# Optimization experiments

Hardware: AMD Instinct MI355X
Metric: run time of the kernel (lower is better)

Reference implementation:

```python
import jax, jax.numpy as jnp
import numpy as np

B, S, D = 2, 2048, 2048
QH, KVH, HD = 32, 8, 64
GRP = QH // KVH  # GQA group size = 4


def setup_inputs() -> dict:
    key = jax.random.key(0)
    ks = jax.random.split(key, 9)
    x = jax.random.normal(ks[0], (B, S, D), jnp.float32)
    # RoPE angle table: [S, HD//2] -> stacked (cos, sin) -> [S, HD//2, 2]
    inv_freq = 1.0 / (10000.0 ** (np.arange(0, HD, 2, dtype=np.float32) / HD))
    ang = np.arange(S, dtype=np.float32)[:, None] * inv_freq[None, :]
    freqs = jnp.stack([jnp.cos(jnp.asarray(ang)), jnp.sin(jnp.asarray(ang))], axis=-1).astype(jnp.float32)
    w = 0.02
    Wq = jax.random.normal(ks[1], (D, QH * HD), jnp.float32) * w
    bq = jnp.zeros((QH * HD,), jnp.float32)
    Wk = jax.random.normal(ks[2], (D, KVH * HD), jnp.float32) * w
    bk = jnp.zeros((KVH * HD,), jnp.float32)
    Wv = jax.random.normal(ks[3], (D, KVH * HD), jnp.float32) * w
    bv = jnp.zeros((KVH * HD,), jnp.float32)
    Wo = jax.random.normal(ks[4], (QH * HD, D), jnp.float32) * w
    bo = jnp.zeros((D,), jnp.float32)
    return {"x": x, "freqs": freqs, "Wq": Wq, "bq": bq, "Wk": Wk, "bk": bk,
            "Wv": Wv, "bv": bv, "Wo": Wo, "bo": bo}


def _rope(xh, cos, sin):
    # xh: [b, s, h, hd]; complex rotation on adjacent pairs, like view_as_complex
    b, s, h, hd = xh.shape
    xp = xh.reshape(b, s, h, hd // 2, 2)
    x0, x1 = xp[..., 0], xp[..., 1]
    o0 = x0 * cos - x1 * sin
    o1 = x0 * sin + x1 * cos
    return jnp.stack([o0, o1], axis=-1).reshape(b, s, h, hd)


def reference(x, freqs, Wq, bq, Wk, bk, Wv, bv, Wo, bo):
    b, s, _ = x.shape
    q = (x @ Wq + bq).reshape(b, s, QH, HD)
    k = (x @ Wk + bk).reshape(b, s, KVH, HD)
    v = (x @ Wv + bv).reshape(b, s, KVH, HD)
    cos = freqs[:s, :, 0][None, :, None, :]  # [1, s, 1, hd//2]
    sin = freqs[:s, :, 1][None, :, None, :]
    q = _rope(q, cos, sin)
    k = _rope(k, cos, sin)
    # [b, h, s, hd]
    q = q.transpose(0, 2, 1, 3).reshape(b, KVH, GRP, s, HD)
    k = k.transpose(0, 2, 1, 3)  # [b, kvh, s, hd]
    v = v.transpose(0, 2, 1, 3)
    scores = jnp.einsum('bkgsh,bkth->bkgst', q, k) / jnp.sqrt(jnp.float32(HD))
    attn = jax.nn.softmax(scores, axis=-1)
    o = jnp.einsum('bkgst,bkth->bkgsh', attn, v)  # [b, kvh, grp, s, hd]
    o = o.reshape(b, QH, s, HD).transpose(0, 2, 1, 3).reshape(b, s, QH * HD)
    return o @ Wo + bo
```

## Files before the change

### kernel.cpp

```cpp
#include <hip/hip_runtime.h>
#include <stdint.h>

#define B_   2
#define S_   2048
#define D_   2048
#define QH_  32
#define KVH_ 8
#define HD_  64

typedef short  short8  __attribute__((ext_vector_type(8)));
typedef float  floatx4 __attribute__((ext_vector_type(4)));

__device__ __forceinline__ ushort f2b(float f) {
  union { float f; uint32_t u; } c; c.f = f;
  uint32_t u = c.u;
  return (ushort)((u + 0x7FFFu + ((u >> 16) & 1u)) >> 16);
}

__device__ __forceinline__ uint32_t fbits(float f) {
  union { float f; uint32_t u; } c; c.f = f;
  return c.u;
}

__device__ __forceinline__ short8 mk8(uint32_t a, uint32_t b, uint32_t c, uint32_t d) {
  union { uint4 u; short8 s; } v; v.u = (uint4){a, b, c, d}; return v.s;
}

__device__ __forceinline__ uint32_t cvtpk(float a, float b) {
  uint32_t r;
  asm("v_cvt_pk_bf16_f32 %0, %1, %2" : "=v"(r) : "v"(a), "v"(b));
  return r;
}

__device__ __forceinline__ void dma16(const void* g, void* l) {
  __builtin_amdgcn_global_load_lds(
      (const __attribute__((address_space(1))) uint32_t*)(uintptr_t)g,
      (__attribute__((address_space(3))) uint32_t*)(uintptr_t)l, 16, 0, 0);
}

#define QSCALE 0.18033688f


__global__ __launch_bounds__(256) void conv_x_kernel(const float* __restrict__ X,
                                                     ushort* __restrict__ Xb) {
  size_t i = ((size_t)blockIdx.x * 256 + threadIdx.x) * 4;
  float4 v = *(const float4*)(X + i);
  ushort4 o;
  o.x = f2b(v.x); o.y = f2b(v.y); o.z = f2b(v.z); o.w = f2b(v.w);
  *(ushort4*)(Xb + i) = o;
}

__global__ void tconv_all_kernel(const float* __restrict__ Wq, const float* __restrict__ Wk,
                                 const float* __restrict__ Wv, const float* __restrict__ Wo,
                                 ushort* __restrict__ wqkv, ushort* __restrict__ wo) {
  __shared__ float tile[32][33];
  int z = blockIdx.z;
  const float* W; ushort* Wt; int N;
  if (z == 0)      { W = Wq; Wt = wqkv;                        N = 2048; }
  else if (z == 1) { W = Wk; Wt = wqkv + (size_t)2048 * 2048;  N = 512;  }
  else if (z == 2) { W = Wv; Wt = wqkv + (size_t)2560 * 2048;  N = 512;  }
  else             { W = Wo; Wt = wo;                          N = 2048; }
  int bx = blockIdx.x, by = blockIdx.y;
  if (bx * 32 >= N) return;
  int tx = threadIdx.x, ty = threadIdx.y;
#pragma unroll
  for (int i = 0; i < 32; i += 8)
    tile[ty + i][tx] = W[(size_t)(by * 32 + ty + i) * N + bx * 32 + tx];
  __syncthreads();
#pragma unroll
  for (int i = 0; i < 32; i += 8)
    Wt[(size_t)(bx * 32 + ty + i) * 2048 + by * 32 + tx] = f2b(tile[tx][ty + i]);
}

__global__ void bias_kernel(const float* __restrict__ bq, const float* __restrict__ bk,
                            const float* __restrict__ bv, float* __restrict__ outb) {
  int i = blockIdx.x * 256 + threadIdx.x;
  if (i >= 3072) return;
  float v;
  if (i < 2048)      v = bq[i];
  else if (i < 2560) v = bk[i - 2048];
  else               v = bv[i - 2560];
  outb[i] = v;
}


__global__ __launch_bounds__(256) void gemm_qkv_kernel(
    const ushort* __restrict__ A, const ushort* __restrict__ Bt,
    const float* __restrict__ bias, const float2* __restrict__ F2,
    ushort* __restrict__ qb, ushort* __restrict__ kb, ushort* __restrict__ vb) {
  const int K = 2048;
  __shared__ ushort sA[2][128 * 32];
  __shared__ ushort sB[2][128 * 32];
  const int tid  = threadIdx.x;
  const int bm   = blockIdx.y, bn = blockIdx.x;
  const int wave = tid >> 6, lane = tid & 63;
  const int quad = lane >> 4, l16 = lane & 15;
  const int wm   = (wave >> 1) * 64, wn = (wave & 1) * 64;

  const ushort* Ab = A  + (size_t)(bm * 128) * K;
  const ushort* Bb = Bt + (size_t)(bn * 128) * K;

  const int gr = lane >> 2;
  const int gu = (lane & 3) * 8;

  floatx4 acc[4][4];
#pragma unroll
  for (int i = 0; i < 4; i++)
#pragma unroll
    for (int j = 0; j < 4; j++) acc[i][j] = (floatx4){0.f, 0.f, 0.f, 0.f};

#pragma unroll
  for (int j = 0; j < 2; j++) {
    int row = j * 64 + wave * 16 + gr;
    dma16(Ab + (size_t)row * K + gu, &sA[0][j * 2048 + wave * 512]);
    dma16(Bb + (size_t)row * K + gu, &sB[0][j * 2048 + wave * 512]);
  }

  int cur = 0;
  for (int k0 = 0; k0 < K; k0 += 32) {
    __syncthreads();
    if (k0 + 32 < K) {
      int nxt = cur ^ 1;
#pragma unroll
      for (int j = 0; j < 2; j++) {
        int row = j * 64 + wave * 16 + gr;
        dma16(Ab + (size_t)row * K + k0 + 32 + gu, &sA[nxt][j * 2048 + wave * 512]);
        dma16(Bb + (size_t)row * K + k0 + 32 + gu, &sB[nxt][j * 2048 + wave * 512]);
      }
    }
    short8 af[4], bf[4];
#pragma unroll
    for (int mi = 0; mi < 4; mi++)
      af[mi] = *(const short8*)&sA[cur][(wm + mi * 16 + l16) * 32 + quad * 8];
#pragma unroll
    for (int ni = 0; ni < 4; ni++)
      bf[ni] = *(const short8*)&sB[cur][(wn + ni * 16 + l16) * 32 + quad * 8];
#pragma unroll
    for (int mi = 0; mi < 4; mi++)
#pragma unroll
      for (int ni = 0; ni < 4; ni++)
        acc[mi][ni] = __builtin_amdgcn_mfma_f32_16x16x32_bf16(
            af[mi], bf[ni], acc[mi][ni], 0, 0, 0);
    cur ^= 1;
  }

  const int isQ = (bn < 16);
  const int isV = (bn >= 20);
  const int hh  = wn >> 6;
  const float sySign = (l16 & 1) ? 1.f : -1.f;
  ushort* dst;
  int hbase;
  if (isQ)      { dst = qb; hbase = bn * 2 + hh; }
  else if (!isV){ dst = kb; hbase = (bn - 16) * 2 + hh; }
  else          { dst = vb; hbase = (bn - 20) * 2 + hh; }
  const int NH = isQ ? QH_ : KVH_;

  float bvv[4];
#pragma unroll
  for (int ni = 0; ni < 4; ni++)
    bvv[ni] = bias[bn * 128 + wn + ni * 16 + l16];

#pragma unroll
  for (int mi = 0; mi < 4; mi++) {
#pragma unroll
    for (int r = 0; r < 4; r++) {
      int row = bm * 128 + wm + mi * 16 + quad * 4 + r;
      int s = row & 2047, bb = row >> 11;
      size_t base = (((size_t)bb * NH + hbase) * S_ + s) * HD_ + l16 * 4;
      ushort4 pk;
      if (!isV) {
        float o[4];
#pragma unroll
        for (int ni = 0; ni < 4; ni++) {
          float xv = acc[mi][ni][r] + bvv[ni];
          float2 cs = F2[s * 32 + ni * 8 + (l16 >> 1)];
          float pp = __shfl_xor(xv, 1);
          float oo = fmaf(pp * sySign, cs.y, xv * cs.x);
          if (isQ) oo *= QSCALE;
          o[ni] = oo;
        }
        pk.x = f2b(o[0]); pk.y = f2b(o[1]); pk.z = f2b(o[2]); pk.w = f2b(o[3]);
      } else {
        pk.x = f2b(acc[mi][0][r] + bvv[0]);
        pk.y = f2b(acc[mi][1][r] + bvv[1]);
        pk.z = f2b(acc[mi][2][r] + bvv[2]);
        pk.w = f2b(acc[mi][3][r] + bvv[3]);
      }
      *(ushort4*)&dst[base] = pk;
    }
  }
}


__global__ __launch_bounds__(256) void gemm_bt_kernel(
    const ushort* __restrict__ A, const ushort* __restrict__ Bt,
    const float* __restrict__ bias, float* __restrict__ C,
    int M, int N, int K) {
  __shared__ ushort sA[2][128 * 32];
  __shared__ ushort sB[2][128 * 32];
  const int tid  = threadIdx.x;
  const int bm   = blockIdx.y, bn = blockIdx.x;
  const int wave = tid >> 6, lane = tid & 63;
  const int quad = lane >> 4, l16 = lane & 15;
  const int wm   = (wave >> 1) * 64, wn = (wave & 1) * 64;

  const ushort* Ab = A  + (size_t)(bm * 128) * K;
  const ushort* Bb = Bt + (size_t)(bn * 128) * K;

  const int gr = lane >> 2;
  const int gu = (lane & 3) * 8;

  floatx4 acc[4][4];
#pragma unroll
  for (int i = 0; i < 4; i++)
#pragma unroll
    for (int j = 0; j < 4; j++) acc[i][j] = (floatx4){0.f, 0.f, 0.f, 0.f};

#pragma unroll
  for (int j = 0; j < 2; j++) {
    int row = j * 64 + wave * 16 + gr;
    dma16(Ab + (size_t)row * K + gu, &sA[0][j * 2048 + wave * 512]);
    dma16(Bb + (size_t)row * K + gu, &sB[0][j * 2048 + wave * 512]);
  }

  int cur = 0;
  for (int k0 = 0; k0 < K; k0 += 32) {
    __syncthreads();
    if (k0 + 32 < K) {
      int nxt = cur ^ 1;
#pragma unroll
      for (int j = 0; j < 2; j++) {
        int row = j * 64 + wave * 16 + gr;
        dma16(Ab + (size_t)row * K + k0 + 32 + gu, &sA[nxt][j * 2048 + wave * 512]);
        dma16(Bb + (size_t)row * K + k0 + 32 + gu, &sB[nxt][j * 2048 + wave * 512]);
      }
    }
    short8 af[4], bf[4];
#pragma unroll
    for (int mi = 0; mi < 4; mi++)
      af[mi] = *(const short8*)&sA[cur][(wm + mi * 16 + l16) * 32 + quad * 8];
#pragma unroll
    for (int ni = 0; ni < 4; ni++)
      bf[ni] = *(const short8*)&sB[cur][(wn + ni * 16 + l16) * 32 + quad * 8];
#pragma unroll
    for (int mi = 0; mi < 4; mi++)
#pragma unroll
      for (int ni = 0; ni < 4; ni++)
        acc[mi][ni] = __builtin_amdgcn_mfma_f32_16x16x32_bf16(
            af[mi], bf[ni], acc[mi][ni], 0, 0, 0);
    cur ^= 1;
  }

#pragma unroll
  for (int mi = 0; mi < 4; mi++) {
#pragma unroll
    for (int ni = 0; ni < 4; ni++) {
      int col  = bn * 128 + wn + ni * 16 + l16;
      float bv = bias[col];
#pragma unroll
      for (int r = 0; r < 4; r++) {
        int row = bm * 128 + wm + mi * 16 + quad * 4 + r;
        C[(size_t)row * N + col] = acc[mi][ni][r] + bv;
      }
    }
  }
}


__global__ void vpack_kernel(const ushort* __restrict__ vb, ushort* __restrict__ Vt) {
  __shared__ ushort tile[64][65];
  int s0 = blockIdx.x * 64;
  int bh = blockIdx.y;
  int tx = threadIdx.x, ty = threadIdx.y;
  int pc = (tx & 32) | ((tx & 12) << 1) | ((tx & 16) >> 2) | (tx & 3);
#pragma unroll
  for (int i = 0; i < 64; i += 8)
    tile[ty + i][tx] = vb[((size_t)bh * S_ + s0 + ty + i) * HD_ + tx];
  __syncthreads();
#pragma unroll
  for (int i = 0; i < 64; i += 8) {
    int dp = ty + i;
    int dt = (dp & 3) * 16 + (dp >> 2);
    Vt[((size_t)bh * HD_ + dt) * S_ + s0 + pc] = tile[tx][dp];
  }
}


__global__ __launch_bounds__(512, 4) void attn_kernel(
    const ushort* __restrict__ Q, const ushort* __restrict__ K,
    const ushort* __restrict__ Vt, ushort* __restrict__ O) {
  const int id  = blockIdx.x + 8 * (blockIdx.y + 32 * blockIdx.z);
  const int kvh = id & 7;
  const int qt  = (id >> 3) & 7;
  const int qh  = kvh * 4 + ((id >> 6) & 3);
  const int b   = id >> 8;
  const int tid = threadIdx.x;
  const int wave = tid >> 6, lane = tid & 63;
  const int quad = lane >> 4, l16 = lane & 15;

  __shared__ ushort kBuf[2][64 * 64];
  __shared__ ushort vBuf[2][64 * 64];

  const ushort* Qh = Q  + ((size_t)(b * QH_ + qh)) * S_ * HD_;
  const ushort* Kh = K  + ((size_t)(b * KVH_ + kvh)) * S_ * HD_;
  const ushort* Vh = Vt + ((size_t)(b * KVH_ + kvh)) * HD_ * S_;

  const int dr = lane >> 3;
  const int du = (lane & 7) ^ (dr & 7);
  const size_t kLaneOff = (size_t)(wave * 8 + dr) * 64 + du * 8;
  const size_t vLaneOff = (size_t)(wave * 8 + dr) * S_ + du * 8;
  const int swz = l16 & 7;

  const int q0 = qt * 256 + wave * 32;
  short8 aq[2][2];
#pragma unroll
  for (int m = 0; m < 2; m++)
#pragma unroll
    for (int s2 = 0; s2 < 2; s2++)
      aq[m][s2] = *(const short8*)(Qh + (size_t)(q0 + m * 16 + l16) * HD_ + s2 * 32 + quad * 8);

  floatx4 oacc[2][4];
#pragma unroll
  for (int m = 0; m < 2; m++)
#pragma unroll
    for (int t = 0; t < 4; t++) oacc[m][t] = (floatx4){0.f, 0.f, 0.f, 0.f};
  float ls[2] = {0.f, 0.f};

  dma16(Kh + kLaneOff, &kBuf[0][wave * 512]);
  dma16(Vh + vLaneOff, &vBuf[0][wave * 512]);

  int cur = 0;
  for (int kv0 = 0; kv0 < S_; kv0 += 64) {
    __syncthreads();
    if (kv0 + 64 < S_) {
      int nxt = cur ^ 1;
      dma16(Kh + (size_t)(kv0 + 64) * 64 + kLaneOff, &kBuf[nxt][wave * 512]);
      dma16(Vh + (size_t)(kv0 + 64) + vLaneOff,      &vBuf[nxt][wave * 512]);
    }

#pragma unroll
    for (int u = 0; u < 2; u++) {
      uint32_t pk[2][4];
#pragma unroll
      for (int cc = 0; cc < 2; cc++) {
        const int c = u * 2 + cc;
        short8 kf0 = *(const short8*)&kBuf[cur][(c * 16 + l16) * 64 + ((quad ^ swz) * 8)];
        short8 kf1 = *(const short8*)&kBuf[cur][(c * 16 + l16) * 64 + (((4 + quad) ^ swz) * 8)];
#pragma unroll
        for (int m = 0; m < 2; m++) {
          floatx4 sc = (floatx4){0.f, 0.f, 0.f, 0.f};
          __builtin_amdgcn_s_setprio(1);
          sc = __builtin_amdgcn_mfma_f32_16x16x32_bf16(kf0, aq[m][0], sc, 0, 0, 0);
          sc = __builtin_amdgcn_mfma_f32_16x16x32_bf16(kf1, aq[m][1], sc, 0, 0, 0);
          __builtin_amdgcn_s_setprio(0);
          float p0 = __builtin_amdgcn_exp2f(sc[0]);
          float p1 = __builtin_amdgcn_exp2f(sc[1]);
          float p2 = __builtin_amdgcn_exp2f(sc[2]);
          float p3 = __builtin_amdgcn_exp2f(sc[3]);
          ls[m] += (p0 + p1) + (p2 + p3);
          pk[m][cc * 2 + 0] = cvtpk(p0, p1);
          pk[m][cc * 2 + 1] = cvtpk(p2, p3);
        }
      }
#pragma unroll
      for (int t = 0; t < 4; t++) {
        const int row = (t * 16 + l16) * 64;
        short8 vf = *(const short8*)&vBuf[cur][row + (((u * 4 + quad) ^ swz) * 8)];
        __builtin_amdgcn_s_setprio(1);
#pragma unroll
        for (int m = 0; m < 2; m++) {
          short8 ap = mk8(pk[m][0], pk[m][1], pk[m][2], pk[m][3]);
          oacc[m][t] = __builtin_amdgcn_mfma_f32_16x16x32_bf16(ap, vf, oacc[m][t], 0, 0, 0);
        }
        __builtin_amdgcn_s_setprio(0);
      }
    }
    cur ^= 1;
  }

#pragma unroll
  for (int m = 0; m < 2; m++) {
    ls[m] += __shfl_xor(ls[m], 16);
    ls[m] += __shfl_xor(ls[m], 32);
  }
#pragma unroll
  for (int m = 0; m < 2; m++) {
#pragma unroll
    for (int r = 0; r < 4; r++) {
      float l = __shfl(ls[m], (lane & 48) | (quad * 4 + r));
      float inv = 1.0f / l;
      int srow = q0 + m * 16 + quad * 4 + r;
      size_t base = ((size_t)b * S_ + srow) * (QH_ * HD_) + (size_t)qh * HD_;
#pragma unroll
      for (int t = 0; t < 4; t++)
        O[base + t * 16 + l16] = f2b(oacc[m][t][r] * inv);
    }
  }
}


extern "C" void kernel_launch(void* const* d_in, const int* in_sizes, int n_in,
                              void* d_out, int out_size, void* d_ws, size_t ws_size,
                              hipStream_t stream) {
  const float* x  = (const float*)d_in[0];
  const float* fr = (const float*)d_in[1];
  const float* Wq = (const float*)d_in[2];
  const float* bq = (const float*)d_in[3];
  const float* Wk = (const float*)d_in[4];
  const float* bk = (const float*)d_in[5];
  const float* Wv = (const float*)d_in[6];
  const float* bv = (const float*)d_in[7];
  const float* Wo = (const float*)d_in[8];
  const float* bo = (const float*)d_in[9];
  float* out = (float*)d_out;
  char* ws = (char*)d_ws;

  ushort* xb    = (ushort*)(ws + 0);
  ushort* wqkv  = (ushort*)(ws + 16777216);
  ushort* wo    = (ushort*)(ws + 29360128);
  float*  biasq = (float* )(ws + 37748736);
  ushort* qb    = (ushort*)(ws + 37761024);
  ushort* kb    = (ushort*)(ws + 54538240);
  ushort* vb    = (ushort*)(ws + 58732544);
  ushort* vt    = (ushort*)(ws + 62926848);
  ushort* ob    = xb;

  conv_x_kernel<<<8192, 256, 0, stream>>>(x, xb);
  tconv_all_kernel<<<dim3(64, 64, 4), dim3(32, 8), 0, stream>>>(Wq, Wk, Wv, Wo, wqkv, wo);
  bias_kernel<<<12, 256, 0, stream>>>(bq, bk, bv, biasq);

  gemm_qkv_kernel<<<dim3(3072 / 128, 4096 / 128), 256, 0, stream>>>(
      xb, wqkv, biasq, (const float2*)fr, qb, kb, vb);

  vpack_kernel<<<dim3(2048 / 64, 16), dim3(64, 8), 0, stream>>>(vb, vt);

  attn_kernel<<<dim3(8, 32, 2), 512, 0, stream>>>(qb, kb, vt, ob);

  gemm_bt_kernel<<<dim3(2048 / 128, 4096 / 128), 256, 0, stream>>>(
      ob, wo, bo, out, 4096, 2048, 2048);
}
```

Measured before the change: 316.1 us.

## Restructure QKV GEMM as 256x256 tile with phased, swizzled LDS pipeline

The QKV projection GEMM now computes a 256x256 output tile per 512-thread block instead of 128x128 per 256-thread block, with K-step 64. Its main loop is an eight-phase schedule that interleaves global-to-LDS DMA for upcoming tiles with MFMA work, using explicit barriers, vmcnt waits and setprio. LDS accesses use an XOR swizzle to avoid bank conflicts. The epilogue is remapped to the new wave layout and writes ushort2 pairs. The goals are more data reuse per block and better overlap of memory and compute, at the cost of more LDS (128 KB), much higher register pressure, and only 192 blocks, which may leave CUs underfilled.

```diff
diff --git a/kernel.cpp b/kernel.cpp
--- a/kernel.cpp
+++ b/kernel.cpp
@@ -84,109 +84,182 @@
 }
 
 
-__global__ __launch_bounds__(256) void gemm_qkv_kernel(
+__global__ __launch_bounds__(512, 2) void gemm_qkv_kernel(
     const ushort* __restrict__ A, const ushort* __restrict__ Bt,
     const float* __restrict__ bias, const float2* __restrict__ F2,
     ushort* __restrict__ qb, ushort* __restrict__ kb, ushort* __restrict__ vb) {
   const int K = 2048;
-  __shared__ ushort sA[2][128 * 32];
-  __shared__ ushort sB[2][128 * 32];
+  __shared__ ushort sA[2][256 * 64];
+  __shared__ ushort sB[2][256 * 64];
   const int tid  = threadIdx.x;
   const int bm   = blockIdx.y, bn = blockIdx.x;
   const int wave = tid >> 6, lane = tid & 63;
   const int quad = lane >> 4, l16 = lane & 15;
-  const int wm   = (wave >> 1) * 64, wn = (wave & 1) * 64;
-
-  const ushort* Ab = A  + (size_t)(bm * 128) * K;
-  const ushort* Bb = Bt + (size_t)(bn * 128) * K;
-
-  const int gr = lane >> 2;
-  const int gu = (lane & 3) * 8;
-
-  floatx4 acc[4][4];
-#pragma unroll
-  for (int i = 0; i < 4; i++)
+  const int wm2  = wave >> 2, wn4 = wave & 3;
+  const int sw7  = l16 & 7;
+  const int dr   = lane >> 3, du = (lane & 7) ^ dr;
+  const int srow = wave * 8 + dr;
+  const int lcol = (lane & 7) * 8;
+
+  const ushort* Ab = A  + (size_t)(bm * 256) * K;
+  const ushort* Bb = Bt + (size_t)(bn * 256) * K;
+
+  floatx4 acc[8][4];
+#pragma unroll
+  for (int i = 0; i < 8; i++)
 #pragma unroll
     for (int j = 0; j < 4; j++) acc[i][j] = (floatx4){0.f, 0.f, 0.f, 0.f};
 
-#pragma unroll
-  for (int j = 0; j < 2; j++) {
-    int row = j * 64 + wave * 16 + gr;
-    dma16(Ab + (size_t)row * K + gu, &sA[0][j * 2048 + wave * 512]);
-    dma16(Bb + (size_t)row * K + gu, &sB[0][j * 2048 + wave * 512]);
-  }
-
-  int cur = 0;
-  for (int k0 = 0; k0 < K; k0 += 32) {
-    __syncthreads();
-    if (k0 + 32 < K) {
-      int nxt = cur ^ 1;
-#pragma unroll
-      for (int j = 0; j < 2; j++) {
-        int row = j * 64 + wave * 16 + gr;
-        dma16(Ab + (size_t)row * K + k0 + 32 + gu, &sA[nxt][j * 2048 + wave * 512]);
-        dma16(Bb + (size_t)row * K + k0 + 32 + gu, &sB[nxt][j * 2048 + wave * 512]);
-      }
-    }
-    short8 af[4], bf[4];
-#pragma unroll
-    for (int mi = 0; mi < 4; mi++)
-      af[mi] = *(const short8*)&sA[cur][(wm + mi * 16 + l16) * 32 + quad * 8];
-#pragma unroll
-    for (int ni = 0; ni < 4; ni++)
-      bf[ni] = *(const short8*)&sB[cur][(wn + ni * 16 + l16) * 32 + quad * 8];
-#pragma unroll
-    for (int mi = 0; mi < 4; mi++)
-#pragma unroll
-      for (int ni = 0; ni < 4; ni++)
-        acc[mi][ni] = __builtin_amdgcn_mfma_f32_16x16x32_bf16(
-            af[mi], bf[ni], acc[mi][ni], 0, 0, 0);
-    cur ^= 1;
-  }
-
-  const int isQ = (bn < 16);
-  const int isV = (bn >= 20);
-  const int hh  = wn >> 6;
+  short8 af[4][2], bf[4][2];
+
+#define STG_A(t, h) do {                                                      \
+    dma16(Ab + (size_t)((h)*128 +      srow) * 2048 + (size_t)(t)*64 + du*8,  \
+          &sA[(t)&1][((h)*128 +      srow) * 64 + lcol]);                     \
+    dma16(Ab + (size_t)((h)*128 + 64 + srow) * 2048 + (size_t)(t)*64 + du*8,  \
+          &sA[(t)&1][((h)*128 + 64 + srow) * 64 + lcol]);                     \
+  } while (0)
+
+#define STG_B(t, h) do {                                                      \
+    dma16(Bb + (size_t)((h)*128 +      srow) * 2048 + (size_t)(t)*64 + du*8,  \
+          &sB[(t)&1][((h)*128 +      srow) * 64 + lcol]);                     \
+    dma16(Bb + (size_t)((h)*128 + 64 + srow) * 2048 + (size_t)(t)*64 + du*8,  \
+          &sB[(t)&1][((h)*128 + 64 + srow) * 64 + lcol]);                     \
+  } while (0)
+
+#define LDA(Sb, mh) do {                                                      \
+    _Pragma("unroll") for (int mi2 = 0; mi2 < 4; mi2++) {                     \
+      const int rr = ((mh)*128 + wm2*64 + mi2*16 + l16) * 64;                 \
+      af[mi2][0] = *(const short8*)&(Sb)[rr + (((quad    ) ^ sw7) * 8)];      \
+      af[mi2][1] = *(const short8*)&(Sb)[rr + (((quad + 4) ^ sw7) * 8)];      \
+    } } while (0)
+
+#define LDB(Sb, nh) do {                                                      \
+    _Pragma("unroll") for (int ni2 = 0; ni2 < 2; ni2++) {                     \
+      const int rr = ((nh)*128 + wn4*32 + ni2*16 + l16) * 64;                 \
+      bf[(nh)*2+ni2][0] = *(const short8*)&(Sb)[rr + (((quad    ) ^ sw7) * 8)]; \
+      bf[(nh)*2+ni2][1] = *(const short8*)&(Sb)[rr + (((quad + 4) ^ sw7) * 8)]; \
+    } } while (0)
+
+#define MFMA_PH(mh, nh) do {                                                  \
+    __builtin_amdgcn_s_setprio(1);                                           \
+    _Pragma("unroll") for (int mi2 = 0; mi2 < 4; mi2++)                       \
+    _Pragma("unroll") for (int ni2 = 0; ni2 < 2; ni2++)                       \
+    _Pragma("unroll") for (int ks = 0; ks < 2; ks++)                          \
+      acc[(mh)*4+mi2][(nh)*2+ni2] = __builtin_amdgcn_mfma_f32_16x16x32_bf16(  \
+        af[mi2][ks], bf[(nh)*2+ni2][ks], acc[(mh)*4+mi2][(nh)*2+ni2], 0,0,0); \
+    __builtin_amdgcn_s_setprio(0);                                            \
+  } while (0)
+
+#define PH_SYNC() do {                                                        \
+    __builtin_amdgcn_sched_barrier(0);                                        \
+    __builtin_amdgcn_s_barrier();                                             \
+    asm volatile("s_waitcnt lgkmcnt(0)" ::: "memory");                        \
+    __builtin_amdgcn_sched_barrier(0);                                        \
+  } while (0)
+
+#define PH_END() do {                                                         \
+    __builtin_amdgcn_sched_barrier(0);                                        \
+    __builtin_amdgcn_s_barrier();                                             \
+    __builtin_amdgcn_sched_barrier(0);                                        \
+  } while (0)
+
+  STG_A(0, 0); STG_A(0, 1); STG_B(0, 0); STG_B(0, 1);
+  STG_A(1, 0); STG_B(1, 0); STG_B(1, 1);
+  asm volatile("s_waitcnt vmcnt(6)" ::: "memory");
+  __builtin_amdgcn_s_barrier();
+
+#pragma unroll 1
+  for (int i = 0; i < 16; ++i) {
+    const int t0 = 2 * i, t1 = 2 * i + 1;
+    const bool more = (i < 15);
+    const ushort* A0 = sA[0]; const ushort* B0 = sB[0];
+    const ushort* A1 = sA[1]; const ushort* B1 = sB[1];
+
+    LDB(B0, 0); LDA(A0, 0);
+    STG_A(t1, 1);
+    PH_SYNC(); MFMA_PH(0, 0); PH_END();
+
+    LDB(B0, 1);
+    if (more) STG_A(t0 + 2, 0);
+    PH_SYNC(); MFMA_PH(0, 1); PH_END();
+
+    LDA(A0, 1);
+    if (more) STG_B(t0 + 2, 0);
+    PH_SYNC(); MFMA_PH(1, 0); PH_END();
+
+    if (more) STG_B(t0 + 2, 1);
+    PH_SYNC(); MFMA_PH(1, 1);
+    if (more) asm volatile("s_waitcnt vmcnt(6)" ::: "memory");
+    else      asm volatile("s_waitcnt vmcnt(0)" ::: "memory");
+    PH_END();
+
+    LDB(B1, 0); LDA(A1, 0);
+    if (more) STG_A(t0 + 2, 1);
+    PH_SYNC(); MFMA_PH(0, 0); PH_END();
+
+    LDB(B1, 1);
+    if (more) STG_A(t1 + 2, 0);
+    PH_SYNC(); MFMA_PH(0, 1); PH_END();
+
+    LDA(A1, 1);
+    if (more) STG_B(t1 + 2, 0);
+    PH_SYNC(); MFMA_PH(1, 0); PH_END();
+
+    if (more) STG_B(t1 + 2, 1);
+    PH_SYNC(); MFMA_PH(1, 1);
+    if (more) asm volatile("s_waitcnt vmcnt(6)" ::: "memory");
+    PH_END();
+  }
+
+#undef STG_A
+#undef STG_B
+#undef LDA
+#undef LDB
+#undef MFMA_PH
+#undef PH_SYNC
+#undef PH_END
+
+  const int isQ = (bn < 8);
+  const int isV = (bn >= 10);
+  ushort* dst = isQ ? qb : (isV ? vb : kb);
+  const int NH   = isQ ? QH_ : KVH_;
+  const int hoff = isQ ? 0 : (isV ? 10 : 8);
   const float sySign = (l16 & 1) ? 1.f : -1.f;
-  ushort* dst;
-  int hbase;
-  if (isQ)      { dst = qb; hbase = bn * 2 + hh; }
-  else if (!isV){ dst = kb; hbase = (bn - 16) * 2 + hh; }
-  else          { dst = vb; hbase = (bn - 20) * 2 + hh; }
-  const int NH = isQ ? QH_ : KVH_;
+  const int dpb = l16 * 4 + (wn4 & 1) * 2;
 
   float bvv[4];
 #pragma unroll
   for (int ni = 0; ni < 4; ni++)
-    bvv[ni] = bias[bn * 128 + wn + ni * 16 + l16];
-
-#pragma unroll
-  for (int mi = 0; mi < 4; mi++) {
+    bvv[ni] = bias[bn * 256 + (ni >> 1) * 128 + wn4 * 32 + (ni & 1) * 16 + l16];
+
+#pragma unroll
+  for (int mi = 0; mi < 8; mi++) {
 #pragma unroll
     for (int r = 0; r < 4; r++) {
-      int row = bm * 128 + wm + mi * 16 + quad * 4 + r;
+      int row = bm * 256 + (mi >> 2) * 128 + wm2 * 64 + (mi & 3) * 16 + quad * 4 + r;
       int s = row & 2047, bb = row >> 11;
-      size_t base = (((size_t)bb * NH + hbase) * S_ + s) * HD_ + l16 * 4;
-      ushort4 pk;
+      float o[4];
       if (!isV) {
-        float o[4];
 #pragma unroll
         for (int ni = 0; ni < 4; ni++) {
           float xv = acc[mi][ni][r] + bvv[ni];
-          float2 cs = F2[s * 32 + ni * 8 + (l16 >> 1)];
+          float2 cs = F2[s * 32 + (wn4 & 1) * 16 + (ni & 1) * 8 + (l16 >> 1)];
           float pp = __shfl_xor(xv, 1);
           float oo = fmaf(pp * sySign, cs.y, xv * cs.x);
           if (isQ) oo *= QSCALE;
           o[ni] = oo;
         }
-        pk.x = f2b(o[0]); pk.y = f2b(o[1]); pk.z = f2b(o[2]); pk.w = f2b(o[3]);
       } else {
-        pk.x = f2b(acc[mi][0][r] + bvv[0]);
-        pk.y = f2b(acc[mi][1][r] + bvv[1]);
-        pk.z = f2b(acc[mi][2][r] + bvv[2]);
-        pk.w = f2b(acc[mi][3][r] + bvv[3]);
+#pragma unroll
+        for (int ni = 0; ni < 4; ni++) o[ni] = acc[mi][ni][r] + bvv[ni];
       }
-      *(ushort4*)&dst[base] = pk;
+#pragma unroll
+      for (int hh = 0; hh < 2; hh++) {
+        int h = (bn - hoff) * 4 + hh * 2 + (wn4 >> 1);
+        size_t base = (((size_t)bb * NH + h) * S_ + s) * HD_ + dpb;
+        ushort2 st; st.x = f2b(o[hh * 2 + 0]); st.y = f2b(o[hh * 2 + 1]);
+        *(ushort2*)&dst[base] = st;
+      }
     }
   }
 }
@@ -429,7 +502,7 @@
   tconv_all_kernel<<<dim3(64, 64, 4), dim3(32, 8), 0, stream>>>(Wq, Wk, Wv, Wo, wqkv, wo);
   bias_kernel<<<12, 256, 0, stream>>>(bq, bk, bv, biasq);
 
-  gemm_qkv_kernel<<<dim3(3072 / 128, 4096 / 128), 256, 0, stream>>>(
+  gemm_qkv_kernel<<<dim3(3072 / 256, 4096 / 256), 512, 0, stream>>>(
       xb, wqkv, biasq, (const float2*)fr, qb, kb, vb);
 
   vpack_kernel<<<dim3(2048 / 64, 16), dim3(64, 8), 0, stream>>>(vb, vt);
```

Result: faster. 309.6 us (-2.0%).

## Fuse V transpose and bias gather into QKV GEMM epilogue; batch attention score MFMAs

Applied to the files above, without the earlier changes.

The QKV GEMM epilogue now writes V straight into the permuted transposed layout the attention kernel reads, so the separate vpack kernel and the intermediate V buffer go away. Biases are read directly from bq/bk/bv, which removes the bias-copy kernel. In the attention loop, all score MFMAs for a 64-key tile are issued together under one priority raise before the exp and PV phases, giving longer MFMA runs. The cost is more live registers for the score fragments and strided, narrow stores in the V epilogue.

```diff
diff --git a/kernel.cpp b/kernel.cpp
--- a/kernel.cpp
+++ b/kernel.cpp
@@ -72,22 +72,12 @@
     Wt[(size_t)(bx * 32 + ty + i) * 2048 + by * 32 + tx] = f2b(tile[tx][ty + i]);
 }
 
-__global__ void bias_kernel(const float* __restrict__ bq, const float* __restrict__ bk,
-                            const float* __restrict__ bv, float* __restrict__ outb) {
-  int i = blockIdx.x * 256 + threadIdx.x;
-  if (i >= 3072) return;
-  float v;
-  if (i < 2048)      v = bq[i];
-  else if (i < 2560) v = bk[i - 2048];
-  else               v = bv[i - 2560];
-  outb[i] = v;
-}
-
 
 __global__ __launch_bounds__(256) void gemm_qkv_kernel(
     const ushort* __restrict__ A, const ushort* __restrict__ Bt,
-    const float* __restrict__ bias, const float2* __restrict__ F2,
-    ushort* __restrict__ qb, ushort* __restrict__ kb, ushort* __restrict__ vb) {
+    const float* __restrict__ bq, const float* __restrict__ bk,
+    const float* __restrict__ bv, const float2* __restrict__ F2,
+    ushort* __restrict__ qb, ushort* __restrict__ kb, ushort* __restrict__ vt) {
   const int K = 2048;
   __shared__ ushort sA[2][128 * 32];
   __shared__ ushort sB[2][128 * 32];
@@ -148,27 +138,26 @@
   const int isV = (bn >= 20);
   const int hh  = wn >> 6;
   const float sySign = (l16 & 1) ? 1.f : -1.f;
-  ushort* dst;
-  int hbase;
-  if (isQ)      { dst = qb; hbase = bn * 2 + hh; }
-  else if (!isV){ dst = kb; hbase = (bn - 16) * 2 + hh; }
-  else          { dst = vb; hbase = (bn - 20) * 2 + hh; }
-  const int NH = isQ ? QH_ : KVH_;
+
+  const float* bsrc = isQ ? bq : (isV ? bv : bk);
+  const int    boff = isQ ? 0  : (isV ? 2560 : 2048);
 
   float bvv[4];
 #pragma unroll
   for (int ni = 0; ni < 4; ni++)
-    bvv[ni] = bias[bn * 128 + wn + ni * 16 + l16];
-
-#pragma unroll
-  for (int mi = 0; mi < 4; mi++) {
-#pragma unroll
-    for (int r = 0; r < 4; r++) {
-      int row = bm * 128 + wm + mi * 16 + quad * 4 + r;
-      int s = row & 2047, bb = row >> 11;
-      size_t base = (((size_t)bb * NH + hbase) * S_ + s) * HD_ + l16 * 4;
-      ushort4 pk;
-      if (!isV) {
+    bvv[ni] = bsrc[bn * 128 + wn + ni * 16 + l16 - boff];
+
+  if (!isV) {
+    ushort* dst = isQ ? qb : kb;
+    const int NH    = isQ ? QH_ : KVH_;
+    const int hbase = isQ ? (bn * 2 + hh) : ((bn - 16) * 2 + hh);
+#pragma unroll
+    for (int mi = 0; mi < 4; mi++) {
+#pragma unroll
+      for (int r = 0; r < 4; r++) {
+        int row = bm * 128 + wm + mi * 16 + quad * 4 + r;
+        int s = row & 2047, bb = row >> 11;
+        size_t base = (((size_t)bb * NH + hbase) * S_ + s) * HD_ + l16 * 4;
         float o[4];
 #pragma unroll
         for (int ni = 0; ni < 4; ni++) {
@@ -179,14 +168,28 @@
           if (isQ) oo *= QSCALE;
           o[ni] = oo;
         }
+        ushort4 pk;
         pk.x = f2b(o[0]); pk.y = f2b(o[1]); pk.z = f2b(o[2]); pk.w = f2b(o[3]);
-      } else {
-        pk.x = f2b(acc[mi][0][r] + bvv[0]);
-        pk.y = f2b(acc[mi][1][r] + bvv[1]);
-        pk.z = f2b(acc[mi][2][r] + bvv[2]);
-        pk.w = f2b(acc[mi][3][r] + bvv[3]);
-      }
-      *(ushort4*)&dst[base] = pk;
+        *(ushort4*)&dst[base] = pk;
+      }
+    }
+  } else {
+    const int h = (bn - 20) * 2 + hh;
+#pragma unroll
+    for (int mi = 0; mi < 4; mi++) {
+      int row0 = bm * 128 + wm + mi * 16 + quad * 4;
+      int bb   = row0 >> 11;
+      int posb = ((row0 & 2047) & ~63) + (mi & 2) * 16 + quad * 8 + (mi & 1) * 4;
+#pragma unroll
+      for (int ni = 0; ni < 4; ni++) {
+        int dt = ni * 16 + l16;
+        ushort4 st;
+        st.x = f2b(acc[mi][ni][0] + bvv[ni]);
+        st.y = f2b(acc[mi][ni][1] + bvv[ni]);
+        st.z = f2b(acc[mi][ni][2] + bvv[ni]);
+        st.w = f2b(acc[mi][ni][3] + bvv[ni]);
+        *(ushort4*)&vt[(((size_t)bb * 8 + h) * 64 + dt) * (size_t)S_ + posb] = st;
+      }
     }
   }
 }
@@ -267,25 +270,6 @@
 }
 
 
-__global__ void vpack_kernel(const ushort* __restrict__ vb, ushort* __restrict__ Vt) {
-  __shared__ ushort tile[64][65];
-  int s0 = blockIdx.x * 64;
-  int bh = blockIdx.y;
-  int tx = threadIdx.x, ty = threadIdx.y;
-  int pc = (tx & 32) | ((tx & 12) << 1) | ((tx & 16) >> 2) | (tx & 3);
-#pragma unroll
-  for (int i = 0; i < 64; i += 8)
-    tile[ty + i][tx] = vb[((size_t)bh * S_ + s0 + ty + i) * HD_ + tx];
-  __syncthreads();
-#pragma unroll
-  for (int i = 0; i < 64; i += 8) {
-    int dp = ty + i;
-    int dt = (dp & 3) * 16 + (dp >> 2);
-    Vt[((size_t)bh * HD_ + dt) * S_ + s0 + pc] = tile[tx][dp];
-  }
-}
-
-
 __global__ __launch_bounds__(512, 4) void attn_kernel(
     const ushort* __restrict__ Q, const ushort* __restrict__ K,
     const ushort* __restrict__ Vt, ushort* __restrict__ O) {
@@ -338,9 +322,10 @@
       dma16(Vh + (size_t)(kv0 + 64) + vLaneOff,      &vBuf[nxt][wave * 512]);
     }
 
+    floatx4 sc[2][2][2];
+    __builtin_amdgcn_s_setprio(1);
 #pragma unroll
     for (int u = 0; u < 2; u++) {
-      uint32_t pk[2][4];
 #pragma unroll
       for (int cc = 0; cc < 2; cc++) {
         const int c = u * 2 + cc;
@@ -348,32 +333,46 @@
         short8 kf1 = *(const short8*)&kBuf[cur][(c * 16 + l16) * 64 + (((4 + quad) ^ swz) * 8)];
 #pragma unroll
         for (int m = 0; m < 2; m++) {
-          floatx4 sc = (floatx4){0.f, 0.f, 0.f, 0.f};
-          __builtin_amdgcn_s_setprio(1);
-          sc = __builtin_amdgcn_mfma_f32_16x16x32_bf16(kf0, aq[m][0], sc, 0, 0, 0);
-          sc = __builtin_amdgcn_mfma_f32_16x16x32_bf16(kf1, aq[m][1], sc, 0, 0, 0);
-          __builtin_amdgcn_s_setprio(0);
-          float p0 = __builtin_amdgcn_exp2f(sc[0]);
-          float p1 = __builtin_amdgcn_exp2f(sc[1]);
-          float p2 = __builtin_amdgcn_exp2f(sc[2]);
-          float p3 = __builtin_amdgcn_exp2f(sc[3]);
+          floatx4 s0 = (floatx4){0.f, 0.f, 0.f, 0.f};
+          s0 = __builtin_amdgcn_mfma_f32_16x16x32_bf16(kf0, aq[m][0], s0, 0, 0, 0);
+          sc[u][cc][m] = __builtin_amdgcn_mfma_f32_16x16x32_bf16(kf1, aq[m][1], s0, 0, 0, 0);
+        }
+      }
+    }
+    __builtin_amdgcn_s_setprio(0);
+
+    uint32_t pk[2][2][4];
+#pragma unroll
+    for (int u = 0; u < 2; u++)
+#pragma unroll
+      for (int cc = 0; cc < 2; cc++)
+#pragma unroll
+        for (int m = 0; m < 2; m++) {
+          float p0 = __builtin_amdgcn_exp2f(sc[u][cc][m][0]);
+          float p1 = __builtin_amdgcn_exp2f(sc[u][cc][m][1]);
+          float p2 = __builtin_amdgcn_exp2f(sc[u][cc][m][2]);
+          float p3 = __builtin_amdgcn_exp2f(sc[u][cc][m][3]);
           ls[m] += (p0 + p1) + (p2 + p3);
-          pk[m][cc * 2 + 0] = cvtpk(p0, p1);
-          pk[m][cc * 2 + 1] = cvtpk(p2, p3);
+          pk[u][m][cc * 2 + 0] = cvtpk(p0, p1);
+          pk[u][m][cc * 2 + 1] = cvtpk(p2, p3);
         }
-      }
+
+#pragma unroll
+    for (int u = 0; u < 2; u++) {
+      short8 ap[2];
+#pragma unroll
+      for (int m = 0; m < 2; m++)
+        ap[m] = mk8(pk[u][m][0], pk[u][m][1], pk[u][m][2], pk[u][m][3]);
+      __builtin_amdgcn_s_setprio(1);
 #pragma unroll
       for (int t = 0; t < 4; t++) {
         const int row = (t * 16 + l16) * 64;
         short8 vf = *(const short8*)&vBuf[cur][row + (((u * 4 + quad) ^ swz) * 8)];
-        __builtin_amdgcn_s_setprio(1);
-#pragma unroll
-        for (int m = 0; m < 2; m++) {
-          short8 ap = mk8(pk[m][0], pk[m][1], pk[m][2], pk[m][3]);
-          oacc[m][t] = __builtin_amdgcn_mfma_f32_16x16x32_bf16(ap, vf, oacc[m][t], 0, 0, 0);
-        }
-        __builtin_amdgcn_s_setprio(0);
-      }
+#pragma unroll
+        for (int m = 0; m < 2; m++)
+          oacc[m][t] = __builtin_amdgcn_mfma_f32_16x16x32_bf16(ap[m], vf, oacc[m][t], 0, 0, 0);
+      }
+      __builtin_amdgcn_s_setprio(0);
     }
     cur ^= 1;
   }
@@ -418,21 +417,16 @@
   ushort* xb    = (ushort*)(ws + 0);
   ushort* wqkv  = (ushort*)(ws + 16777216);
   ushort* wo    = (ushort*)(ws + 29360128);
-  float*  biasq = (float* )(ws + 37748736);
   ushort* qb    = (ushort*)(ws + 37761024);
   ushort* kb    = (ushort*)(ws + 54538240);
-  ushort* vb    = (ushort*)(ws + 58732544);
   ushort* vt    = (ushort*)(ws + 62926848);
   ushort* ob    = xb;
 
   conv_x_kernel<<<8192, 256, 0, stream>>>(x, xb);
   tconv_all_kernel<<<dim3(64, 64, 4), dim3(32, 8), 0, stream>>>(Wq, Wk, Wv, Wo, wqkv, wo);
-  bias_kernel<<<12, 256, 0, stream>>>(bq, bk, bv, biasq);
 
   gemm_qkv_kernel<<<dim3(3072 / 128, 4096 / 128), 256, 0, stream>>>(
-      xb, wqkv, biasq, (const float2*)fr, qb, kb, vb);
-
-  vpack_kernel<<<dim3(2048 / 64, 16), dim3(64, 8), 0, stream>>>(vb, vt);
+      xb, wqkv, bq, bk, bv, (const float2*)fr, qb, kb, vt);
 
   attn_kernel<<<dim3(8, 32, 2), 512, 0, stream>>>(qb, kb, vt, ob);
 
```

New measurement: 323.3 us. +2.3%, slower.
